# Performance work log

Measured on AMD Instinct MI355X. Metric: run time of the kernel, lower is better.

The kernel has to match this reference:

```python
import math
import jax, jax.numpy as jnp
import numpy as np

B, S, D, H = 2, 2048, 1024, 16
HD = D // H  # 64
EPS = 1e-5


def _layernorm(x, g, b):
    mu = jnp.mean(x, axis=-1, keepdims=True)
    var = jnp.mean(jnp.square(x - mu), axis=-1, keepdims=True)
    return (x - mu) * jax.lax.rsqrt(var + EPS) * g + b


def setup_inputs() -> dict:
    key = jax.random.key(0)
    ks = jax.random.split(key, 16)
    s_attn = 1.0 / math.sqrt(D)
    s_mlp = 1.0 / math.sqrt(4 * D)
    return {
        "hidden_states": jax.random.normal(ks[0], (B, S, D), jnp.float32),
        # MHA params (torch Linear convention: y = x @ W.T + b)
        "Wqkv": jax.random.normal(ks[1], (3 * D, D), jnp.float32) * s_attn,
        "bqkv": jax.random.normal(ks[2], (3 * D,), jnp.float32) * s_attn,
        "Wout": jax.random.normal(ks[3], (D, D), jnp.float32) * s_attn,
        "bout": jax.random.normal(ks[4], (D,), jnp.float32) * s_attn,
        # LayerNorms
        "g1": jnp.ones((D,), jnp.float32),
        "b1": jnp.zeros((D,), jnp.float32),
        "g2": jnp.ones((D,), jnp.float32),
        "b2": jnp.zeros((D,), jnp.float32),
        # MLP (hidden = 4*D, activation = tanh)
        "W1": jax.random.normal(ks[5], (4 * D, D), jnp.float32) * s_attn,
        "bfc1": jax.random.normal(ks[6], (4 * D,), jnp.float32) * s_attn,
        "W2": jax.random.normal(ks[7], (D, 4 * D), jnp.float32) * s_mlp,
        "bfc2": jax.random.normal(ks[8], (D,), jnp.float32) * s_mlp,
    }


def _mha(x, Wqkv, bqkv, Wout, bout):
    # qkv: (B,S,3,H,hd)
    qkv = (x @ Wqkv.T + bqkv).reshape(B, S, 3, H, HD)
    q, k, v = qkv[:, :, 0], qkv[:, :, 1], qkv[:, :, 2]
    # NOTE: source einsum 'bshd,btjd->bsht' contracts over k's head axis j,
    # so each query head attends against sum-over-heads of K (and of V).
    k_sum = k.sum(axis=2)  # (B,S,hd)
    v_sum = v.sum(axis=2)  # (B,S,hd)
    scale = 1.0 / math.sqrt(HD)
    scores = jnp.einsum('bshd,btd->bsht', q, k_sum) * scale  # (B,S,H,S)
    causal = jnp.triu(jnp.ones((S, S), bool), k=1)  # True above diagonal
    scores = jnp.where(causal[None, :, None, :], -jnp.inf, scores)
    attn = jax.nn.softmax(scores, axis=-1)
    out = jnp.einsum('bsht,btd->bshd', attn, v_sum).reshape(B, S, D)
    return out @ Wout.T + bout


def reference(hidden_states, Wqkv, bqkv, Wout, bout, g1, b1, g2, b2, W1, bfc1, W2, bfc2):
    # eval mode: dropouts and stochastic-depth are identity
    residual = hidden_states
    h = _layernorm(residual, g1, b1)
    h = _mha(h, Wqkv, bqkv, Wout, bout)
    residual = h + residual
    h = _layernorm(residual, g2, b2)
    h = jnp.tanh(h @ W1.T + bfc1) @ W2.T + bfc2
    return (h, residual)
```

## Files before the change

kernel.cpp:

```cpp
#include <hip/hip_runtime.h>
#include <hip/hip_bf16.h>

typedef __attribute__((ext_vector_type(8))) short s16x8;
typedef __attribute__((ext_vector_type(4))) float f32x4;
typedef __hip_bfloat16 bf16_t;

__device__ __forceinline__ void gload_lds16(const void* g, void* l) {
  __builtin_amdgcn_global_load_lds(
      (__attribute__((address_space(1))) void*)(g),
      (__attribute__((address_space(3))) void*)(l), 16, 0, 0);
}

__device__ __forceinline__ unsigned cvt_pk_bf16(float lo, float hi) {
  unsigned r;
  asm("v_cvt_pk_bf16_f32 %0, %1, %2" : "=v"(r) : "v"(lo), "v"(hi));
  return r;
}

__device__ __forceinline__ float fast_tanh(float x) {
  float t = exp2f(x * 2.885390082f);
  return 1.0f - 2.0f * __builtin_amdgcn_rcpf(t + 1.0f);
}

__global__ void cast_all_k(const float* __restrict__ Wqkv, const float* __restrict__ Wout,
                           const float* __restrict__ W1, const float* __restrict__ W2,
                           bf16_t* __restrict__ Wqkv_bf, bf16_t* __restrict__ Wout_bf,
                           bf16_t* __restrict__ W1_bf, bf16_t* __restrict__ W2_bf) {
  int c = blockIdx.x * 256 + threadIdx.x;
  const float* src; bf16_t* dst; int off;
  if (c < 131072)      { src = Wqkv; dst = Wqkv_bf; off = c; }
  else if (c < 262144) { src = Wout; dst = Wout_bf; off = c - 131072; }
  else if (c < 786432) { src = W1;   dst = W1_bf;   off = c - 262144; }
  else                 { src = W2;   dst = W2_bf;   off = c - 786432; }
  int i = off * 8;
  float4 a = *(const float4*)(src + i);
  float4 b = *(const float4*)(src + i + 4);
  union { bf16_t h[8]; s16x8 v; } u;
  u.h[0] = __float2bfloat16(a.x); u.h[1] = __float2bfloat16(a.y);
  u.h[2] = __float2bfloat16(a.z); u.h[3] = __float2bfloat16(a.w);
  u.h[4] = __float2bfloat16(b.x); u.h[5] = __float2bfloat16(b.y);
  u.h[6] = __float2bfloat16(b.z); u.h[7] = __float2bfloat16(b.w);
  *(s16x8*)(dst + i) = u.v;
}

__global__ void reduce_kv_k(const float* __restrict__ Wqkv, bf16_t* __restrict__ Wred) {
  int d   = blockIdx.x & 63;
  int isv = blockIdx.x >> 6;
  int col = threadIdx.x * 4;
  const float* base = Wqkv + (size_t)(1024 + isv * 1024 + d) * 1024 + col;
  float4 s = {0.f, 0.f, 0.f, 0.f};
#pragma unroll
  for (int h = 0; h < 16; ++h) {
    float4 t = *(const float4*)(base + (size_t)h * 64 * 1024);
    s.x += t.x; s.y += t.y; s.z += t.z; s.w += t.w;
  }
  union { bf16_t h[4]; uint2 u; } o;
  o.h[0] = __float2bfloat16(s.x); o.h[1] = __float2bfloat16(s.y);
  o.h[2] = __float2bfloat16(s.z); o.h[3] = __float2bfloat16(s.w);
  *(uint2*)(Wred + (size_t)(isv * 64 + d) * 1024 + col) = o.u;
}

__global__ void bias_prep_k(const float* __restrict__ bqkv, float* __restrict__ br) {
  int i = blockIdx.x * 256 + threadIdx.x;
  if (i >= 1152) return;
  if (i < 1024) { br[i] = bqkv[i]; return; }
  int d = i - 1024;
  int off = (d < 64) ? (1024 + d) : (2048 + (d - 64));
  float s = 0.f;
#pragma unroll
  for (int h = 0; h < 16; ++h) s += bqkv[off + h * 64];
  br[i] = s;
}

__global__ __launch_bounds__(256) void ln_cast_k(const float* __restrict__ x,
                                                 const float* __restrict__ g,
                                                 const float* __restrict__ bb,
                                                 bf16_t* __restrict__ y) {
  int row = blockIdx.x, tid = threadIdx.x;
  float4 v = *(const float4*)(x + (size_t)row * 1024 + tid * 4);
  float s = v.x + v.y + v.z + v.w;
  float q = v.x * v.x + v.y * v.y + v.z * v.z + v.w * v.w;
#pragma unroll
  for (int off = 1; off < 64; off <<= 1) {
    s += __shfl_xor(s, off, 64);
    q += __shfl_xor(q, off, 64);
  }
  __shared__ float ss[4], qq[4];
  int wave = tid >> 6, lane = tid & 63;
  if (lane == 0) { ss[wave] = s; qq[wave] = q; }
  __syncthreads();
  s = ss[0] + ss[1] + ss[2] + ss[3];
  q = qq[0] + qq[1] + qq[2] + qq[3];
  float mu  = s * (1.0f / 1024.0f);
  float var = q * (1.0f / 1024.0f) - mu * mu;
  float rstd = rsqrtf(var + 1e-5f);
  float4 gg = *(const float4*)(g + tid * 4);
  float4 bv = *(const float4*)(bb + tid * 4);
  union { bf16_t h[4]; uint2 u; } o;
  o.h[0] = __float2bfloat16((v.x - mu) * rstd * gg.x + bv.x);
  o.h[1] = __float2bfloat16((v.y - mu) * rstd * gg.y + bv.y);
  o.h[2] = __float2bfloat16((v.z - mu) * rstd * gg.z + bv.z);
  o.h[3] = __float2bfloat16((v.w - mu) * rstd * gg.w + bv.w);
  *(uint2*)(y + (size_t)row * 1024 + tid * 4) = o.u;
}

template <int EPI>
__global__ __launch_bounds__(512) void gemm256(
    const bf16_t* __restrict__ A, const bf16_t* __restrict__ Bw,
    const float* __restrict__ bias, void* __restrict__ out0,
    int M, int N, int K, int Kslice) {
  __shared__ __align__(16) bf16_t As[3 * 8192];
  __shared__ __align__(16) bf16_t Bs[3 * 8192];
  const int tid  = threadIdx.x;
  const int lane = tid & 63;
  const int wave = tid >> 6;
  const int l15 = lane & 15, lg = lane >> 4;
  const int wm = wave >> 2, wn = wave & 3;
  const int bm = blockIdx.y * 256, bn = blockIdx.x * 256;
  const size_t Kz = (size_t)K;
  const int kstart = blockIdx.z * Kslice;
  const int srow = lane >> 2;
  const int scol = ((lane & 3) ^ ((lane >> 3) & 3)) * 8;
  const int rdoff = (lg ^ ((l15 >> 1) & 3)) * 8;

  f32x4 acc[8][4];
#pragma unroll
  for (int f = 0; f < 8; ++f)
#pragma unroll
    for (int g = 0; g < 4; ++g) acc[f][g] = (f32x4){0.f, 0.f, 0.f, 0.f};

  const bf16_t* Ab = A + (size_t)bm * Kz + kstart;
  const bf16_t* Bb = Bw + (size_t)bn * Kz + kstart;

  auto stage = [&](int t, int buf) {
    const int k0 = t * 32;
#pragma unroll
    for (int j = 0; j < 2; ++j) {
      const int blk = wave * 2 + j;
      gload_lds16(Ab + (size_t)(blk * 16 + srow) * Kz + k0 + scol, As + buf * 8192 + blk * 512);
      gload_lds16(Bb + (size_t)(blk * 16 + srow) * Kz + k0 + scol, Bs + buf * 8192 + blk * 512);
    }
  };

  const int NT = Kslice >> 5;
  stage(0, 0);
  stage(1, 1);
  int b0 = 0, b1 = 1, b2 = 2;
  for (int t = 0; t < NT; ++t) {
    if (t + 1 < NT) asm volatile("s_waitcnt vmcnt(4)" ::: "memory");
    else            asm volatile("s_waitcnt vmcnt(0)" ::: "memory");
    __builtin_amdgcn_s_barrier();
    if (t + 2 < NT) stage(t + 2, b2);
    s16x8 af[8], bfv[4];
#pragma unroll
    for (int f = 0; f < 8; ++f)
      af[f] = *(const s16x8*)&As[b0 * 8192 + (wm * 128 + f * 16 + l15) * 32 + rdoff];
#pragma unroll
    for (int g = 0; g < 4; ++g)
      bfv[g] = *(const s16x8*)&Bs[b0 * 8192 + (wn * 64 + g * 16 + l15) * 32 + rdoff];
    __builtin_amdgcn_s_setprio(1);
#pragma unroll
    for (int f = 0; f < 8; ++f)
#pragma unroll
      for (int g = 0; g < 4; ++g)
        acc[f][g] = __builtin_amdgcn_mfma_f32_16x16x32_bf16(af[f], bfv[g], acc[f][g], 0, 0, 0);
    __builtin_amdgcn_s_setprio(0);
    int tmp = b0; b0 = b1; b1 = b2; b2 = tmp;
  }

#pragma unroll
  for (int f = 0; f < 8; ++f) {
    const int row0 = bm + wm * 128 + f * 16 + lg * 4;
#pragma unroll
    for (int g = 0; g < 4; ++g) {
      const int col = bn + wn * 64 + g * 16 + l15;
      const float bcol = (EPI == 4) ? 0.f : bias[col];
#pragma unroll
      for (int r = 0; r < 4; ++r) {
        const int rw = row0 + r;
        float c = acc[f][g][r] + bcol;
        if constexpr (EPI == 2) {
          ((bf16_t*)out0)[(size_t)rw * N + col] = __float2bfloat16(fast_tanh(c));
        } else {
          ((bf16_t*)out0)[((size_t)blockIdx.z * M + rw) * N + col] = __float2bfloat16(c);
        }
      }
    }
  }
}

template <int EPI>
__global__ __launch_bounds__(256) void gemm64(
    const bf16_t* __restrict__ A, const bf16_t* __restrict__ Bw,
    const float* __restrict__ bias, void* __restrict__ out0,
    const float* __restrict__ resid, bf16_t* __restrict__ oks,
    bf16_t* __restrict__ ovt, int M, int N, int K) {
  __shared__ __align__(16) bf16_t As[2 * 64 * 32];
  __shared__ __align__(16) bf16_t Bs[2 * 128 * 32];
  const int tid  = threadIdx.x;
  const int lane = tid & 63;
  const int wave = tid >> 6;
  const int l15 = lane & 15, lg = lane >> 4;
  const int wr = (wave >> 1) * 32, wc = (wave & 1) * 64;
  const int bm = blockIdx.y * 64, bn = blockIdx.x * 128;
  const size_t Kz = (size_t)K;
  const int srow = lane >> 2;
  const int scol = ((lane & 3) ^ ((lane >> 3) & 3)) * 8;

  f32x4 acc[2][4];
#pragma unroll
  for (int m = 0; m < 2; ++m)
#pragma unroll
    for (int n = 0; n < 4; ++n) acc[m][n] = (f32x4){0.f, 0.f, 0.f, 0.f};

  const bf16_t* Ab = A + (size_t)bm * Kz;
  const bf16_t* Bb = Bw + (size_t)bn * Kz;

  auto stage = [&](int t, int buf) {
    const int k0 = t * 32;
    gload_lds16(Ab + (size_t)(wave * 16 + srow) * Kz + k0 + scol, As + buf * 2048 + wave * 512);
#pragma unroll
    for (int j = 0; j < 2; ++j) {
      const int cw = wave * 2 + j;
      gload_lds16(Bb + (size_t)(cw * 16 + srow) * Kz + k0 + scol, Bs + buf * 4096 + cw * 512);
    }
  };

  const int NT = K >> 5;
  const int rdoff = (lg ^ ((l15 >> 1) & 3)) * 8;
  stage(0, 0);
  __syncthreads();
  int buf = 0;
  for (int t = 0; t < NT; ++t) {
    if (t + 1 < NT) stage(t + 1, buf ^ 1);
    s16x8 af[2], bfv[4];
#pragma unroll
    for (int m = 0; m < 2; ++m)
      af[m] = *(const s16x8*)&As[buf * 2048 + (wr + m * 16 + l15) * 32 + rdoff];
#pragma unroll
    for (int n = 0; n < 4; ++n)
      bfv[n] = *(const s16x8*)&Bs[buf * 4096 + (wc + n * 16 + l15) * 32 + rdoff];
#pragma unroll
    for (int m = 0; m < 2; ++m)
#pragma unroll
      for (int n = 0; n < 4; ++n)
        acc[m][n] = __builtin_amdgcn_mfma_f32_16x16x32_bf16(af[m], bfv[n], acc[m][n], 0, 0, 0);
    __syncthreads();
    buf ^= 1;
  }

#pragma unroll
  for (int m = 0; m < 2; ++m) {
    const int row0 = bm + wr + m * 16 + lg * 4;
#pragma unroll
    for (int n = 0; n < 4; ++n) {
      const int col = bn + wc + n * 16 + l15;
      const float bcol = bias[col];
#pragma unroll
      for (int r = 0; r < 4; ++r) {
        const int rw = row0 + r;
        float c = acc[m][n][r] + bcol;
        if constexpr (EPI == 0) {
          if (col < 1024) {
            ((bf16_t*)out0)[(size_t)rw * 1024 + col] = __float2bfloat16(c);
          } else if (col < 1088) {
            int d = col - 1024, b = rw >> 11, t = rw & 2047;
            oks[((size_t)(b << 11) + t) * 64 + d] = __float2bfloat16(c);
          } else {
            int d = col - 1088, b = rw >> 11, t = rw & 2047;
            ovt[((size_t)b * 64 + d) * 2048 + t] = __float2bfloat16(c);
          }
        } else {
          ((float*)out0)[(size_t)rw * N + col] = c + resid[(size_t)rw * N + col];
        }
      }
    }
  }
}

__global__ __launch_bounds__(256) void fc2_reduce_k(const bf16_t* __restrict__ p,
                                                    const float* __restrict__ bias,
                                                    float* __restrict__ out) {
  const size_t PL = (size_t)4096 * 1024;
  size_t i = ((size_t)blockIdx.x * 256 + threadIdx.x) * 8;
  float acc[8];
  {
    union { s16x8 v; bf16_t h[8]; } u;
    u.v = *(const s16x8*)(p + i);
#pragma unroll
    for (int j = 0; j < 8; ++j) acc[j] = __bfloat162float(u.h[j]);
  }
#pragma unroll
  for (int z = 1; z < 4; ++z) {
    union { s16x8 v; bf16_t h[8]; } u;
    u.v = *(const s16x8*)(p + z * PL + i);
#pragma unroll
    for (int j = 0; j < 8; ++j) acc[j] += __bfloat162float(u.h[j]);
  }
  const int col = (int)(i & 1023);
#pragma unroll
  for (int j = 0; j < 8; ++j) acc[j] += bias[col + j];
  *(float4*)(out + i)     = (float4){acc[0], acc[1], acc[2], acc[3]};
  *(float4*)(out + i + 4) = (float4){acc[4], acc[5], acc[6], acc[7]};
}

template <bool MASK>
__device__ __forceinline__ void attn_tile(
    int t0, int p, const s16x8 (&qf)[2],
    const bf16_t* __restrict__ Ks, const bf16_t* __restrict__ Vs,
    bf16_t* __restrict__ Pl, int l15, int lg,
    float& m_run, float& l_part, f32x4 (&ao)[4]) {
  constexpr float SCL = 0.125f * 1.44269504088896f;
  const int sw7 = l15 & 7;

  f32x4 sc[4];
#pragma unroll
  for (int n = 0; n < 4; ++n) sc[n] = (f32x4){0.f, 0.f, 0.f, 0.f};
#pragma unroll
  for (int ks2 = 0; ks2 < 2; ++ks2) {
#pragma unroll
    for (int n = 0; n < 4; ++n) {
      s16x8 kf = *(const s16x8*)&Ks[(n * 16 + l15) * 64 + (((ks2 << 2) | lg) ^ sw7) * 8];
      sc[n] = __builtin_amdgcn_mfma_f32_16x16x32_bf16(kf, qf[ks2], sc[n], 0, 0, 0);
    }
  }

  float mx = -1e30f;
#pragma unroll
  for (int n = 0; n < 4; ++n) {
#pragma unroll
    for (int r = 0; r < 4; ++r) {
      float v = sc[n][r] * SCL;
      if (MASK && (t0 + n * 16 + lg * 4 + r > p)) v = -1e30f;
      sc[n][r] = v;
      mx = fmaxf(mx, v);
    }
  }
  if (__any(mx > m_run + 11.5f)) {
    float mxf = fmaxf(mx, __shfl_xor(mx, 16, 64));
    mxf = fmaxf(mxf, __shfl_xor(mxf, 32, 64));
    float mn = fmaxf(m_run, mxf);
    float alpha = exp2f(m_run - mn);
    m_run = mn;
    l_part *= alpha;
#pragma unroll
    for (int r = 0; r < 4; ++r) {
      float ar = __shfl(alpha, lg * 4 + r, 64);
#pragma unroll
      for (int n2 = 0; n2 < 4; ++n2) ao[n2][r] *= ar;
    }
  }
#pragma unroll
  for (int n = 0; n < 4; ++n) {
    float e0 = exp2f(sc[n][0] - m_run);
    float e1 = exp2f(sc[n][1] - m_run);
    float e2 = exp2f(sc[n][2] - m_run);
    float e3 = exp2f(sc[n][3] - m_run);
    l_part += (e0 + e1) + (e2 + e3);
    uint2 d;
    d.x = cvt_pk_bf16(e0, e1);
    d.y = cvt_pk_bf16(e2, e3);
    *(uint2*)&Pl[l15 * 72 + n * 16 + lg * 4] = d;
  }
#pragma unroll
  for (int ks2 = 0; ks2 < 2; ++ks2) {
    s16x8 pa = *(const s16x8*)&Pl[l15 * 72 + ks2 * 32 + lg * 8];
#pragma unroll
    for (int n2 = 0; n2 < 4; ++n2) {
      s16x8 vf = *(const s16x8*)&Vs[(n2 * 16 + l15) * 64 + (((ks2 << 2) | lg) ^ sw7) * 8];
      ao[n2] = __builtin_amdgcn_mfma_f32_16x16x32_bf16(pa, vf, ao[n2], 0, 0, 0);
    }
  }
}

__global__ __launch_bounds__(512) void attn_k(const bf16_t* __restrict__ q,
                                              const bf16_t* __restrict__ ksp,
                                              const bf16_t* __restrict__ vtp,
                                              bf16_t* __restrict__ o) {
  __shared__ __align__(16) bf16_t Ks[64 * 64];
  __shared__ __align__(16) bf16_t Vs[64 * 64];
  __shared__ __align__(16) bf16_t Plds[8][16 * 72];
  const int tid = threadIdx.x, lane = tid & 63, wave = tid >> 6;
  const int l15 = lane & 15, lg = lane >> 4;
  const int grp = blockIdx.x >> 1;
  const int b   = blockIdx.x & 1;
  const int pbase = 2040 - 8 * grp;
  const int p = pbase + wave;

  const bf16_t* qb_b = q   + (size_t)b * 32768 * 64;
  const bf16_t* ksb  = ksp + (size_t)b * 2048 * 64;
  const bf16_t* vtb  = vtp + (size_t)b * 64 * 2048;
  bf16_t*       ob   = o   + (size_t)b * 32768 * 64;
  bf16_t* Pl = &Plds[wave][0];

  const int srow = lane >> 3;
  const int scol = lane & 7;
  const int grow = wave * 8 + srow;
  const int gcol = scol ^ (grow & 7);
  const bf16_t* ksrc0 = ksb + (size_t)grow * 64 + gcol * 8;
  const bf16_t* vsrc0 = vtb + (size_t)grow * 2048 + gcol * 8;
  bf16_t* kdst = Ks + wave * 512;
  bf16_t* vdst = Vs + wave * 512;

  s16x8 qf[2];
  {
    const bf16_t* qptr = qb_b + (size_t)(16 * p + l15) * 64;
    qf[0] = *(const s16x8*)(qptr + lg * 8);
    qf[1] = *(const s16x8*)(qptr + 32 + lg * 8);
  }

  float m_run = -1e30f, l_part = 0.f;
  f32x4 ao[4];
#pragma unroll
  for (int n = 0; n < 4; ++n) ao[n] = (f32x4){0.f, 0.f, 0.f, 0.f};

  const int nsteps = (pbase + 71) >> 6;
  for (int tt = 0; tt < nsteps; ++tt) {
    const int t0 = tt * 64;
    __syncthreads();
    gload_lds16(ksrc0 + (size_t)t0 * 64, kdst);
    gload_lds16(vsrc0 + t0, vdst);
    __syncthreads();
    if (t0 <= p) {
      if (t0 + 63 <= p)
        attn_tile<false>(t0, p, qf, Ks, Vs, Pl, l15, lg, m_run, l_part, ao);
      else
        attn_tile<true>(t0, p, qf, Ks, Vs, Pl, l15, lg, m_run, l_part, ao);
    }
  }

  float l2 = l_part + __shfl_xor(l_part, 16, 64);
  l2 += __shfl_xor(l2, 32, 64);
  float rl[4];
#pragma unroll
  for (int r = 0; r < 4; ++r) rl[r] = 1.0f / __shfl(l2, lg * 4 + r, 64);
#pragma unroll
  for (int n2 = 0; n2 < 4; ++n2) {
#pragma unroll
    for (int r = 0; r < 4; ++r) {
      const int row = 16 * p + lg * 4 + r;
      ob[(size_t)row * 64 + n2 * 16 + l15] = __float2bfloat16(ao[n2][r] * rl[r]);
    }
  }
}

extern "C" void kernel_launch(void* const* d_in, const int* in_sizes, int n_in,
                              void* d_out, int out_size, void* d_ws, size_t ws_size,
                              hipStream_t stream) {
  (void)in_sizes; (void)n_in; (void)out_size; (void)ws_size;
  const float* hidden = (const float*)d_in[0];
  const float* Wqkv   = (const float*)d_in[1];
  const float* bqkv   = (const float*)d_in[2];
  const float* Wout   = (const float*)d_in[3];
  const float* bout   = (const float*)d_in[4];
  const float* g1     = (const float*)d_in[5];
  const float* b1     = (const float*)d_in[6];
  const float* g2     = (const float*)d_in[7];
  const float* b2     = (const float*)d_in[8];
  const float* W1     = (const float*)d_in[9];
  const float* bfc1   = (const float*)d_in[10];
  const float* W2     = (const float*)d_in[11];
  const float* bfc2   = (const float*)d_in[12];

  float* out_h   = (float*)d_out;
  float* out_res = out_h + (size_t)4096 * 1024;

  char* ws = (char*)d_ws;
  auto alloc = [&](size_t bytes) {
    char* p = ws;
    ws += (bytes + 255) & ~(size_t)255;
    return p;
  };
  bf16_t* X1      = (bf16_t*)alloc((size_t)4096 * 1024 * 2);
  bf16_t* Wqkv_bf = (bf16_t*)alloc((size_t)1152 * 1024 * 2);
  float*  bias_r  = (float*)alloc(1152 * 4);
  bf16_t* qb      = (bf16_t*)alloc((size_t)4096 * 1024 * 2);
  bf16_t* ksum    = (bf16_t*)alloc((size_t)2 * 2048 * 64 * 2);
  bf16_t* vT      = (bf16_t*)alloc((size_t)2 * 64 * 2048 * 2);
  bf16_t* Ob      = (bf16_t*)alloc((size_t)4096 * 1024 * 2);
  bf16_t* Wout_bf = (bf16_t*)alloc((size_t)1024 * 1024 * 2);
  bf16_t* X2      = (bf16_t*)alloc((size_t)4096 * 1024 * 2);
  bf16_t* W1_bf   = (bf16_t*)alloc((size_t)4096 * 1024 * 2);
  bf16_t* W2_bf   = (bf16_t*)alloc((size_t)1024 * 4096 * 2);
  bf16_t* H1      = (bf16_t*)alloc((size_t)4096 * 4096 * 2);
  bf16_t* fc2_part = (bf16_t*)d_ws;

  cast_all_k<<<5120, 256, 0, stream>>>(Wqkv, Wout, W1, W2, Wqkv_bf, Wout_bf, W1_bf, W2_bf);
  reduce_kv_k<<<128, 256, 0, stream>>>(Wqkv, Wqkv_bf + (size_t)1024 * 1024);
  bias_prep_k<<<5, 256, 0, stream>>>(bqkv, bias_r);

  ln_cast_k<<<4096, 256, 0, stream>>>(hidden, g1, b1, X1);
  gemm64<0><<<dim3(9, 64), 256, 0, stream>>>(X1, Wqkv_bf, bias_r, qb, nullptr, ksum, vT,
                                             4096, 1152, 1024);
  attn_k<<<512, 512, 0, stream>>>(qb, ksum, vT, Ob);
  gemm64<1><<<dim3(8, 64), 256, 0, stream>>>(Ob, Wout_bf, bout, out_res, hidden, nullptr,
                                             nullptr, 4096, 1024, 1024);
  ln_cast_k<<<4096, 256, 0, stream>>>(out_res, g2, b2, X2);
  gemm256<2><<<dim3(16, 16), 512, 0, stream>>>(X2, W1_bf, bfc1, H1, 4096, 4096, 1024, 1024);
  gemm256<4><<<dim3(4, 16, 4), 512, 0, stream>>>(H1, W2_bf, nullptr, fc2_part,
                                                 4096, 1024, 4096, 1024);
  fc2_reduce_k<<<2048, 256, 0, stream>>>(fc2_part, bfc2, out_h);
}
```

Measured before the change: 233.5 us.

## Triple-buffer K/V tiles in attention and fold softmax scale into Q

The attention kernel now keeps three LDS buffers for K and V tiles and issues async global-to-LDS loads two tiles ahead. It synchronizes with vmcnt waits and a single barrier per step, replacing the two __syncthreads per iteration. The softmax scale times log2(e) is moved into the QKV GEMM epilogue, which removes a multiply per score. The cost is three times the LDS for K/V and a reliance on vmcnt counting matching exactly two outstanding loads per stage.

```diff
diff --git a/kernel.cpp b/kernel.cpp
--- a/kernel.cpp
+++ b/kernel.cpp
@@ -262,7 +262,8 @@
         float c = acc[m][n][r] + bcol;
         if constexpr (EPI == 0) {
           if (col < 1024) {
-            ((bf16_t*)out0)[(size_t)rw * 1024 + col] = __float2bfloat16(c);
+            ((bf16_t*)out0)[(size_t)rw * 1024 + col] =
+                __float2bfloat16(c * 0.1803368801f);
           } else if (col < 1088) {
             int d = col - 1024, b = rw >> 11, t = rw & 2047;
             oks[((size_t)(b << 11) + t) * 64 + d] = __float2bfloat16(c);
@@ -304,13 +305,13 @@
   *(float4*)(out + i + 4) = (float4){acc[4], acc[5], acc[6], acc[7]};
 }
 
+
 template <bool MASK>
 __device__ __forceinline__ void attn_tile(
     int t0, int p, const s16x8 (&qf)[2],
     const bf16_t* __restrict__ Ks, const bf16_t* __restrict__ Vs,
     bf16_t* __restrict__ Pl, int l15, int lg,
     float& m_run, float& l_part, f32x4 (&ao)[4]) {
-  constexpr float SCL = 0.125f * 1.44269504088896f;
   const int sw7 = l15 & 7;
 
   f32x4 sc[4];
@@ -330,7 +331,7 @@
   for (int n = 0; n < 4; ++n) {
 #pragma unroll
     for (int r = 0; r < 4; ++r) {
-      float v = sc[n][r] * SCL;
+      float v = sc[n][r];
       if (MASK && (t0 + n * 16 + lg * 4 + r > p)) v = -1e30f;
       sc[n][r] = v;
       mx = fmaxf(mx, v);
@@ -377,8 +378,8 @@
                                               const bf16_t* __restrict__ ksp,
                                               const bf16_t* __restrict__ vtp,
                                               bf16_t* __restrict__ o) {
-  __shared__ __align__(16) bf16_t Ks[64 * 64];
-  __shared__ __align__(16) bf16_t Vs[64 * 64];
+  __shared__ __align__(16) bf16_t Ks[3 * 4096];
+  __shared__ __align__(16) bf16_t Vs[3 * 4096];
   __shared__ __align__(16) bf16_t Plds[8][16 * 72];
   const int tid = threadIdx.x, lane = tid & 63, wave = tid >> 6;
   const int l15 = lane & 15, lg = lane >> 4;
@@ -399,8 +400,12 @@
   const int gcol = scol ^ (grow & 7);
   const bf16_t* ksrc0 = ksb + (size_t)grow * 64 + gcol * 8;
   const bf16_t* vsrc0 = vtb + (size_t)grow * 2048 + gcol * 8;
-  bf16_t* kdst = Ks + wave * 512;
-  bf16_t* vdst = Vs + wave * 512;
+
+  auto stageKV = [&](int t, int buf) {
+    const int t0 = t * 64;
+    gload_lds16(ksrc0 + (size_t)t0 * 64, Ks + buf * 4096 + wave * 512);
+    gload_lds16(vsrc0 + t0, Vs + buf * 4096 + wave * 512);
+  };
 
   s16x8 qf[2];
   {
@@ -414,19 +419,25 @@
 #pragma unroll
   for (int n = 0; n < 4; ++n) ao[n] = (f32x4){0.f, 0.f, 0.f, 0.f};
 
-  const int nsteps = (pbase + 71) >> 6;
-  for (int tt = 0; tt < nsteps; ++tt) {
+  const int nst = (pbase + 71) >> 6;
+  stageKV(0, 0);
+  if (nst > 1) stageKV(1, 1);
+  int b0 = 0, b1 = 1, b2 = 2;
+  for (int tt = 0; tt < nst; ++tt) {
+    if (tt + 1 < nst) asm volatile("s_waitcnt vmcnt(2)" ::: "memory");
+    else              asm volatile("s_waitcnt vmcnt(0)" ::: "memory");
+    __builtin_amdgcn_s_barrier();
+    if (tt + 2 < nst) stageKV(tt + 2, b2);
     const int t0 = tt * 64;
-    __syncthreads();
-    gload_lds16(ksrc0 + (size_t)t0 * 64, kdst);
-    gload_lds16(vsrc0 + t0, vdst);
-    __syncthreads();
     if (t0 <= p) {
+      const bf16_t* Kc = Ks + b0 * 4096;
+      const bf16_t* Vc = Vs + b0 * 4096;
       if (t0 + 63 <= p)
-        attn_tile<false>(t0, p, qf, Ks, Vs, Pl, l15, lg, m_run, l_part, ao);
+        attn_tile<false>(t0, p, qf, Kc, Vc, Pl, l15, lg, m_run, l_part, ao);
       else
-        attn_tile<true>(t0, p, qf, Ks, Vs, Pl, l15, lg, m_run, l_part, ao);
-    }
+        attn_tile<true>(t0, p, qf, Kc, Vc, Pl, l15, lg, m_run, l_part, ao);
+    }
+    int tmp = b0; b0 = b1; b1 = b2; b2 = tmp;
   }
 
   float l2 = l_part + __shfl_xor(l_part, 16, 64);
```

Measured after the change: 228.1 us, median of 2. -2.3%, faster.
